# Performance work log

Hardware: AMD Instinct MI355X
Metric: run time of the kernel (lower is better)

## Reference

```python
import jax, jax.numpy as jnp
import numpy as np

EPS = 1e-5

def _rmsnorm(x, g):
    xf = x.astype(jnp.float32)
    rms = jnp.sqrt(jnp.mean(xf * xf + EPS, axis=-1, keepdims=True))
    return (xf / rms * g).astype(x.dtype)

def setup_inputs() -> dict:
    key = jax.random.key(0)
    ks = jax.random.split(key, 10)
    B, S, D, H, F = 2, 2048, 1024, 16, 4096
    s = 0.02
    return {
        "x": jax.random.normal(ks[0], (B, S, D), jnp.float32),
        "g1": jnp.ones((D,), jnp.float32),
        "wq": jax.random.normal(ks[1], (D, D), jnp.float32) * s,
        "wk": jax.random.normal(ks[2], (D, D), jnp.float32) * s,
        "wv": jax.random.normal(ks[3], (D, D), jnp.float32) * s,
        "wo": jax.random.normal(ks[4], (D, D), jnp.float32) * s,
        "g2": jnp.ones((D,), jnp.float32),
        "w1": jax.random.normal(ks[5], (F, D), jnp.float32) * s,
        "w2": jax.random.normal(ks[6], (D, F), jnp.float32) * s,
        "w3": jax.random.normal(ks[7], (F, D), jnp.float32) * s,
    }

def reference(x, g1, wq, wk, wv, wo, g2, w1, w2, w3):
    B, S, D = x.shape
    H = 16
    hd = D // H
    # --- attention sublayer ---
    xn = _rmsnorm(x, g1)
    q = jnp.einsum('bsd,ed->bse', xn, wq).reshape(B, S, H, hd).transpose(0, 2, 1, 3)
    k = jnp.einsum('bsd,ed->bse', xn, wk).reshape(B, S, H, hd).transpose(0, 2, 1, 3)
    v = jnp.einsum('bsd,ed->bse', xn, wv).reshape(B, S, H, hd).transpose(0, 2, 1, 3)
    scores = jnp.einsum('bhqd,bhkd->bhqk', q, k) / jnp.sqrt(jnp.float32(hd))
    mask = jnp.tril(jnp.ones((S, S), bool))  # causal
    neg = jnp.finfo(scores.dtype).min
    scores = jnp.where(mask[None, None], scores, neg)
    probs = jax.nn.softmax(scores, axis=-1)
    o = jnp.einsum('bhqk,bhkd->bhqd', probs, v)
    o = o.transpose(0, 2, 1, 3).reshape(B, S, D)
    attn_out = jnp.einsum('bsv,dv->bsd', o, wo)
    h = x + attn_out
    # --- SwiGLU sublayer ---
    hn = _rmsnorm(h, g2)
    p1 = jnp.einsum('fd,bsd->bsf', w1, hn)
    p3 = jnp.einsum('fd,bsd->bsf', w3, hn)
    ffn = jnp.einsum('df,bsf->bsd', w2, jax.nn.silu(p1) * p3)
    return h + ffn
```

## Files before the change

### kernel.cpp

```cpp
#include <hip/hip_runtime.h>

typedef __attribute__((ext_vector_type(8))) short short8;
typedef __attribute__((ext_vector_type(4))) float f32x4;

__device__ __forceinline__ unsigned short f2b(float f) {
  union { float f; unsigned u; } v; v.f = f;
  unsigned r = v.u + 0x7fffu + ((v.u >> 16) & 1u);
  return (unsigned short)(r >> 16);
}
__device__ __forceinline__ float b2f(unsigned short b) {
  union { unsigned u; float f; } v; v.u = ((unsigned)b) << 16; return v.f;
}

__device__ __forceinline__ void gload_lds16(const void* g, void* l) {
  __builtin_amdgcn_global_load_lds(
      (const __attribute__((address_space(1))) void*)g,
      (__attribute__((address_space(3))) void*)l, 16, 0, 0);
}

__global__ __launch_bounds__(256) void cvt_k(const float* __restrict__ s,
                                             unsigned short* __restrict__ d, int n4) {
  int i = blockIdx.x * 256 + threadIdx.x;
  if (i >= n4) return;
  float4 v = ((const float4*)s)[i];
  ushort4 o;
  o.x = f2b(v.x); o.y = f2b(v.y); o.z = f2b(v.z); o.w = f2b(v.w);
  ((ushort4*)d)[i] = o;
}

__global__ __launch_bounds__(256) void rmsnorm_k(const float* __restrict__ x,
                                                 const float* __restrict__ g,
                                                 unsigned short* __restrict__ out) {
  const int row = blockIdx.x, tid = threadIdx.x;
  const float4 v = ((const float4*)(x + (size_t)row * 1024))[tid];
  float ss = v.x*v.x + v.y*v.y + v.z*v.z + v.w*v.w;
  #pragma unroll
  for (int d = 32; d > 0; d >>= 1) ss += __shfl_down(ss, d);
  __shared__ float red[4];
  if ((tid & 63) == 0) red[tid >> 6] = ss;
  __syncthreads();
  const float tot = red[0] + red[1] + red[2] + red[3];
  const float sc = rsqrtf(tot * (1.0f/1024.0f) + 1e-5f);
  const float4 gg = ((const float4*)g)[tid];
  ushort4 o;
  o.x = f2b(v.x * sc * gg.x); o.y = f2b(v.y * sc * gg.y);
  o.z = f2b(v.z * sc * gg.z); o.w = f2b(v.w * sc * gg.w);
  ((ushort4*)(out + (size_t)row * 1024))[tid] = o;
}

__global__ __launch_bounds__(256) void gate_k(unsigned short* __restrict__ p13) {
  const size_t i = (size_t)blockIdx.x * 256 + threadIdx.x;
  const int r = (int)(i >> 9);
  const int fc = ((int)i & 511) * 8;
  unsigned short* p1 = p13 + (size_t)r * 8192 + fc;
  const unsigned short* p3 = p13 + (size_t)r * 8192 + 4096 + fc;
  ushort4 a0 = ((const ushort4*)p1)[0], a1 = ((const ushort4*)p1)[1];
  ushort4 b0 = ((const ushort4*)p3)[0], b1 = ((const ushort4*)p3)[1];
  unsigned short va[8] = {a0.x,a0.y,a0.z,a0.w,a1.x,a1.y,a1.z,a1.w};
  unsigned short vb[8] = {b0.x,b0.y,b0.z,b0.w,b1.x,b1.y,b1.z,b1.w};
  unsigned short vo[8];
  #pragma unroll
  for (int j = 0; j < 8; ++j) {
    float f1 = b2f(va[j]), f3 = b2f(vb[j]);
    float s = f1 / (1.0f + __expf(-f1));
    vo[j] = f2b(s * f3);
  }
  ushort4 o0 = {vo[0],vo[1],vo[2],vo[3]}, o1 = {vo[4],vo[5],vo[6],vo[7]};
  ((ushort4*)p1)[0] = o0; ((ushort4*)p1)[1] = o1;
}

template<int EPI>
__global__ __launch_bounds__(256) void gemm_bt(
    const unsigned short* __restrict__ A, const unsigned short* __restrict__ W,
    int N, int K, int lda,
    unsigned short* __restrict__ Cb, const float* __restrict__ res,
    float* __restrict__ Cf, int ldc)
{
  __shared__ unsigned short sA[4096];
  __shared__ unsigned short sB[4096];
  const int tid = threadIdx.x;
  const int w = tid >> 6, l = tid & 63;
  const int l15 = l & 15, l4 = l >> 4;
  const int bm = blockIdx.y * 128, bn = blockIdx.x * 128;
  const int wm = (w >> 1) * 64, wn = (w & 1) * 64;
  const int c0 = w * 128 + l;
  const int ra0 = c0 >> 2,        ka0 = (c0 & 3) * 8;
  const int ra1 = (c0 + 64) >> 2, ka1 = ((c0 + 64) & 3) * 8;
  const unsigned short* Ar0 = A + (size_t)(bm + ra0) * lda + ka0;
  const unsigned short* Ar1 = A + (size_t)(bm + ra1) * lda + ka1;
  const unsigned short* Wr0 = W + (size_t)(bn + ra0) * K + ka0;
  const unsigned short* Wr1 = W + (size_t)(bn + ra1) * K + ka1;
  f32x4 acc[4][4];
  const f32x4 z4 = {0.f, 0.f, 0.f, 0.f};
  #pragma unroll
  for (int i = 0; i < 4; ++i)
    #pragma unroll
    for (int j = 0; j < 4; ++j) acc[i][j] = z4;

  for (int kt = 0; kt < K; kt += 32) {
    gload_lds16(Ar0 + kt, &sA[w * 1024]);
    gload_lds16(Ar1 + kt, &sA[w * 1024 + 512]);
    gload_lds16(Wr0 + kt, &sB[w * 1024]);
    gload_lds16(Wr1 + kt, &sB[w * 1024 + 512]);
    __syncthreads();
    short8 af[4], bf[4];
    #pragma unroll
    for (int mi = 0; mi < 4; ++mi)
      af[mi] = *(const short8*)&sA[(wm + mi*16 + l15)*32 + l4*8];
    #pragma unroll
    for (int ni = 0; ni < 4; ++ni)
      bf[ni] = *(const short8*)&sB[(wn + ni*16 + l15)*32 + l4*8];
    #pragma unroll
    for (int mi = 0; mi < 4; ++mi)
      #pragma unroll
      for (int ni = 0; ni < 4; ++ni)
        acc[mi][ni] = __builtin_amdgcn_mfma_f32_16x16x32_bf16(af[mi], bf[ni], acc[mi][ni], 0, 0, 0);
    __syncthreads();
  }
  #pragma unroll
  for (int mi = 0; mi < 4; ++mi)
    #pragma unroll
    for (int ni = 0; ni < 4; ++ni) {
      const int row0 = bm + wm + mi*16 + l4*4;
      const int col  = bn + wn + ni*16 + l15;
      #pragma unroll
      for (int r = 0; r < 4; ++r) {
        const float v = acc[mi][ni][r];
        if (EPI == 0) {
          Cb[(size_t)(row0 + r) * ldc + col] = f2b(v);
        } else {
          const size_t o = (size_t)(row0 + r) * ldc + col;
          Cf[o] = res[o] + v;
        }
      }
    }
}

__global__ __launch_bounds__(256) void vtrans_k(const unsigned short* __restrict__ QKV,
                                                unsigned short* __restrict__ VT) {
  __shared__ unsigned short sT[4096];
  const int st = blockIdx.x, dt = blockIdx.y, b = blockIdx.z;
  const int tid = threadIdx.x;
  #pragma unroll
  for (int half = 0; half < 2; ++half) {
    const int c = tid + half * 256;
    const int r = c >> 3;
    const int ch = c & 7;
    const unsigned short* src =
        QKV + (size_t)(b*2048 + st*64 + r) * 3072 + 2048 + dt*64 + ch*8;
    short8 v = *(const short8*)src;
    *(short8*)&sT[r*64 + ((ch ^ ((r >> 3) & 7)) * 8)] = v;
  }
  __syncthreads();
  #pragma unroll
  for (int half = 0; half < 2; ++half) {
    const int c = tid + half * 256;
    const int od = c >> 3;
    const int oc = c & 7;
    unsigned short tmp[8];
    #pragma unroll
    for (int j = 0; j < 8; ++j) {
      const int srow = oc*8 + j;
      const int chunk = (od >> 3) ^ ((srow >> 3) & 7);
      tmp[j] = sT[srow*64 + chunk*8 + (od & 7)];
    }
    *(short8*)&VT[(size_t)(b*1024 + dt*64 + od) * 2048 + st*64 + oc*8] = *(short8*)tmp;
  }
}

__global__ __launch_bounds__(256) void attn_k(const unsigned short* __restrict__ QKV,
                                              const unsigned short* __restrict__ VT,
                                              unsigned short* __restrict__ Ob)
{
  const int LDQ = 3072;
  const int b = blockIdx.y >> 4, h = blockIdx.y & 15;
  const int qb = (15 - (int)blockIdx.x) * 128;
  const int tid = threadIdx.x;
  const int w = tid >> 6, l = tid & 63;
  const int l15 = l & 15, l4 = l >> 4;
  const int qw = qb + w * 32;
  const unsigned short* Qg  = QKV + (size_t)(b * 2048) * LDQ + h * 64;
  const unsigned short* Kg  = Qg + 1024;
  const unsigned short* VTg = VT + (size_t)(b * 1024 + h * 64) * 2048;

  __shared__ unsigned short sK[2][4096];
  __shared__ unsigned short sVT[2][4096];
  __shared__ unsigned short sP[4][2304];

  short8 qf[2][2];
  #pragma unroll
  for (int qt = 0; qt < 2; ++qt)
    #pragma unroll
    for (int hc = 0; hc < 2; ++hc)
      qf[qt][hc] = *(const short8*)&Qg[(size_t)(qw + qt*16 + l15) * LDQ + hc*32 + l4*8];

  const int rc0 = tid >> 3;
  const int ch0 = (tid & 7) ^ (rc0 & 7);
  const int rc1 = rc0 + 32;
  const unsigned short* Ks0 = Kg  + (size_t)rc0 * LDQ  + ch0 * 8;
  const unsigned short* Ks1 = Kg  + (size_t)rc1 * LDQ  + ch0 * 8;
  const unsigned short* Vs0 = VTg + (size_t)rc0 * 2048 + ch0 * 8;
  const unsigned short* Vs1 = VTg + (size_t)rc1 * 2048 + ch0 * 8;
  const int wun0 = w * 512;
  const int wun1 = 2048 + w * 512;

  f32x4 accO[2][4];
  float m_run[2][4], l_run[2][4];
  const f32x4 z4 = {0.f,0.f,0.f,0.f};
  #pragma unroll
  for (int qt = 0; qt < 2; ++qt) {
    #pragma unroll
    for (int dt = 0; dt < 4; ++dt) accO[qt][dt] = z4;
    #pragma unroll
    for (int r = 0; r < 4; ++r) { m_run[qt][r] = -1e30f; l_run[qt][r] = 0.f; }
  }

  const int ntB = (qb >> 6) + 2;
#define ASTAGE(buf, t) do { \
    const size_t ko = (size_t)(t) * 64 * LDQ; const int vo = (t) * 64; \
    gload_lds16(Ks0 + ko, &sK[buf][wun0]); \
    gload_lds16(Ks1 + ko, &sK[buf][wun1]); \
    gload_lds16(Vs0 + vo, &sVT[buf][wun0]); \
    gload_lds16(Vs1 + vo, &sVT[buf][wun1]); } while (0)

  ASTAGE(0, 0);
  __syncthreads();
  int cur = 0;
  for (int t = 0; t < ntB; ++t) {
    if (t + 1 < ntB) ASTAGE(cur ^ 1, t + 1);
    const int kv = t * 64;
    if (kv <= qw + 31) {
      const unsigned short* Kb = sK[cur];
      const unsigned short* Vb = sVT[cur];
      const int lim = qw + 31 - kv;
      f32x4 sAcc[2][4];
      #pragma unroll
      for (int qt = 0; qt < 2; ++qt)
        #pragma unroll
        for (int nt = 0; nt < 4; ++nt) sAcc[qt][nt] = z4;
      #pragma unroll
      for (int nt = 0; nt < 4; ++nt) {
        if (nt * 16 <= lim) {
          const int krow = nt*16 + l15;
          const short8 kf0 = *(const short8*)&Kb[krow*64 + ((l4 ^ (krow & 7)) * 8)];
          const short8 kf1 = *(const short8*)&Kb[krow*64 + (((4 + l4) ^ (krow & 7)) * 8)];
          #pragma unroll
          for (int qt = 0; qt < 2; ++qt) {
            sAcc[qt][nt] = __builtin_amdgcn_mfma_f32_16x16x32_bf16(qf[qt][0], kf0, sAcc[qt][nt], 0,0,0);
            sAcc[qt][nt] = __builtin_amdgcn_mfma_f32_16x16x32_bf16(qf[qt][1], kf1, sAcc[qt][nt], 0,0,0);
          }
        }
      }
      const bool bound = (kv + 63 > qw);
      #pragma unroll
      for (int qt = 0; qt < 2; ++qt) {
        float fac[4]; bool resc_any = false;
        #pragma unroll
        for (int r = 0; r < 4; ++r) {
          float sv[4];
          #pragma unroll
          for (int nt = 0; nt < 4; ++nt)
            sv[nt] = (nt * 16 <= lim) ? sAcc[qt][nt][r] * 0.125f : -1e30f;
          if (bound) {
            const int row = qt*16 + l4*4 + r;
            #pragma unroll
            for (int nt = 0; nt < 4; ++nt)
              if (kv + nt*16 + l15 > qw + row) sv[nt] = -1e30f;
          }
          float mx = fmaxf(fmaxf(sv[0], sv[1]), fmaxf(sv[2], sv[3]));
          mx = fmaxf(mx, __shfl_xor(mx, 1));
          mx = fmaxf(mx, __shfl_xor(mx, 2));
          mx = fmaxf(mx, __shfl_xor(mx, 4));
          mx = fmaxf(mx, __shfl_xor(mx, 8));
          const float mo = m_run[qt][r];
          const bool resc = mx > mo + 8.0f;
          const float mn = resc ? mx : mo;
          const float f = resc ? __expf(mo - mn) : 1.0f;
          fac[r] = f; resc_any |= resc;
          const float p0 = __expf(sv[0]-mn), p1 = __expf(sv[1]-mn);
          const float p2 = __expf(sv[2]-mn), p3 = __expf(sv[3]-mn);
          float rs = (p0+p1)+(p2+p3);
          rs += __shfl_xor(rs,1); rs += __shfl_xor(rs,2);
          rs += __shfl_xor(rs,4); rs += __shfl_xor(rs,8);
          l_run[qt][r] = l_run[qt][r]*f + rs;
          m_run[qt][r] = mn;
          const int prow = qt*16 + l4*4 + r;
          sP[w][prow*72      + l15] = f2b(p0);
          sP[w][prow*72 + 16 + l15] = f2b(p1);
          sP[w][prow*72 + 32 + l15] = f2b(p2);
          sP[w][prow*72 + 48 + l15] = f2b(p3);
        }
        if (__any(resc_any)) {
          #pragma unroll
          for (int dt = 0; dt < 4; ++dt)
            #pragma unroll
            for (int r = 0; r < 4; ++r)
              accO[qt][dt][r] *= fac[r];
        }
      }
      short8 pf[2][2];
      #pragma unroll
      for (int qt = 0; qt < 2; ++qt)
        #pragma unroll
        for (int kc = 0; kc < 2; ++kc)
          pf[qt][kc] = *(const short8*)&sP[w][(qt*16 + l15)*72 + kc*32 + l4*8];
      #pragma unroll
      for (int dt = 0; dt < 4; ++dt) {
        const int vrow = dt*16 + l15;
        const short8 vf0 = *(const short8*)&Vb[vrow*64 + ((l4 ^ (vrow & 7)) * 8)];
        const short8 vf1 = *(const short8*)&Vb[vrow*64 + (((4 + l4) ^ (vrow & 7)) * 8)];
        #pragma unroll
        for (int qt = 0; qt < 2; ++qt) {
          accO[qt][dt] = __builtin_amdgcn_mfma_f32_16x16x32_bf16(pf[qt][0], vf0, accO[qt][dt], 0,0,0);
          accO[qt][dt] = __builtin_amdgcn_mfma_f32_16x16x32_bf16(pf[qt][1], vf1, accO[qt][dt], 0,0,0);
        }
      }
    }
    __syncthreads();
    cur ^= 1;
  }
  #pragma unroll
  for (int qt = 0; qt < 2; ++qt)
    #pragma unroll
    for (int dt = 0; dt < 4; ++dt)
      #pragma unroll
      for (int r = 0; r < 4; ++r) {
        const int row = qw + qt*16 + l4*4 + r;
        const float ov = accO[qt][dt][r] / l_run[qt][r];
        Ob[(size_t)(b*2048 + row) * 1024 + h*64 + dt*16 + l15] = f2b(ov);
      }
}

extern "C" void kernel_launch(void* const* d_in, const int* in_sizes, int n_in,
                              void* d_out, int out_size, void* d_ws, size_t ws_size,
                              hipStream_t stream) {
  const float* x  = (const float*)d_in[0];
  const float* g1 = (const float*)d_in[1];
  const float* wq = (const float*)d_in[2];
  const float* wk = (const float*)d_in[3];
  const float* wv = (const float*)d_in[4];
  const float* wo = (const float*)d_in[5];
  const float* g2 = (const float*)d_in[6];
  const float* w1 = (const float*)d_in[7];
  const float* w2 = (const float*)d_in[8];
  const float* w3 = (const float*)d_in[9];
  float* out = (float*)d_out;
  char* ws = (char*)d_ws;
  (void)in_sizes; (void)n_in; (void)out_size; (void)ws_size;

  unsigned short* Wqkv = (unsigned short*)(ws + 0);
  unsigned short* Wo   = (unsigned short*)(ws + 6291456);
  unsigned short* W13  = (unsigned short*)(ws + 8388608);
  unsigned short* W2   = (unsigned short*)(ws + 25165824);
  unsigned short* XN   = (unsigned short*)(ws + 33554432);
  unsigned short* QKV  = (unsigned short*)(ws + 41943040);
  unsigned short* OB   = (unsigned short*)(ws + 67108864);
  unsigned short* VTb  = (unsigned short*)(ws + 75497472);
  unsigned short* P13  = (unsigned short*)(ws + 41943040);
  float*          H    = (float*)(ws + 109051904);

  cvt_k<<<1024, 256, 0, stream>>>(wq, Wqkv,             262144);
  cvt_k<<<1024, 256, 0, stream>>>(wk, Wqkv + 1048576,   262144);
  cvt_k<<<1024, 256, 0, stream>>>(wv, Wqkv + 2097152,   262144);
  cvt_k<<<1024, 256, 0, stream>>>(wo, Wo,               262144);
  cvt_k<<<4096, 256, 0, stream>>>(w1, W13,             1048576);
  cvt_k<<<4096, 256, 0, stream>>>(w3, W13 + 4194304,   1048576);
  cvt_k<<<4096, 256, 0, stream>>>(w2, W2,              1048576);

  rmsnorm_k<<<4096, 256, 0, stream>>>(x, g1, XN);
  gemm_bt<0><<<dim3(24, 32), 256, 0, stream>>>(XN, Wqkv, 3072, 1024, 1024,
                                               QKV, nullptr, nullptr, 3072);
  vtrans_k<<<dim3(32, 16, 2), 256, 0, stream>>>(QKV, VTb);
  attn_k<<<dim3(16, 32), 256, 0, stream>>>(QKV, VTb, OB);
  gemm_bt<1><<<dim3(8, 32), 256, 0, stream>>>(OB, Wo, 1024, 1024, 1024,
                                              nullptr, x, H, 1024);
  rmsnorm_k<<<4096, 256, 0, stream>>>(H, g2, XN);
  gemm_bt<0><<<dim3(64, 32), 256, 0, stream>>>(XN, W13, 8192, 1024, 1024,
                                               P13, nullptr, nullptr, 8192);
  gate_k<<<8192, 256, 0, stream>>>(P13);
  gemm_bt<1><<<dim3(8, 32), 256, 0, stream>>>(P13, W2, 1024, 4096, 8192,
                                              nullptr, H, out, 1024);
}
```

Before: 571.1 us.

## Add 256x256-tile 4-stage pipelined bf16 GEMM for QKV and W1/W3 projections

```diff
diff --git a/kernel.cpp b/kernel.cpp
--- a/kernel.cpp
+++ b/kernel.cpp
@@ -134,6 +134,113 @@
         }
       }
     }
+}
+
+__global__ __launch_bounds__(512, 2) void gemm256_bt(
+    const unsigned short* __restrict__ A, const unsigned short* __restrict__ W,
+    int K, int lda, unsigned short* __restrict__ Cb, int ldc, int nbx)
+{
+  __shared__ unsigned short sA[4][8192];
+  __shared__ unsigned short sB[4][8192];
+  const int tid = threadIdx.x;
+  const int w = tid >> 6, l = tid & 63;
+  const int l15 = l & 15, l4 = l >> 4;
+  const int nwg = nbx * gridDim.y;
+  const int flat = blockIdx.y * nbx + blockIdx.x;
+  const int q8 = nwg >> 3;
+  const int sw = (flat & 7) * q8 + (flat >> 3);
+  const int bm = (sw / nbx) * 256, bn = (sw % nbx) * 256;
+
+  int rowl[2], coll[2];
+  #pragma unroll
+  for (int i = 0; i < 2; ++i) {
+    const int g = w * 128 + i * 64 + l;
+    const int s = g >> 6, j = g & 63;
+    const int r = j >> 2, c8 = (j & 3) * 8;
+    rowl[i] = s * 16 + r;
+    coll[i] = c8 ^ ((r & 8) << 1);
+  }
+  const unsigned short* As0 = A + (size_t)(bm + rowl[0]) * lda + coll[0];
+  const unsigned short* As1 = A + (size_t)(bm + rowl[1]) * lda + coll[1];
+  const unsigned short* Ws0 = W + (size_t)(bn + rowl[0]) * K + coll[0];
+  const unsigned short* Ws1 = W + (size_t)(bn + rowl[1]) * K + coll[1];
+  const int d0 = w * 1024, d1 = w * 1024 + 512;
+
+  const int swzr = (l4 * 8) ^ ((l15 & 8) << 1);
+  const int aoff = (w >> 2) * 4096 + l15 * 32 + swzr;
+  const int boff = (w & 3) * 2048 + l15 * 32 + swzr;
+
+  f32x4 acc[8][4];
+  const f32x4 z4 = {0.f, 0.f, 0.f, 0.f};
+  #pragma unroll
+  for (int i = 0; i < 8; ++i)
+    #pragma unroll
+    for (int j = 0; j < 4; ++j) acc[i][j] = z4;
+
+  const int NT = K >> 5;
+  #pragma unroll
+  for (int p = 0; p < 3; ++p) {
+    const int ko = p * 32;
+    gload_lds16(As0 + ko, &sA[p][d0]);
+    gload_lds16(As1 + ko, &sA[p][d1]);
+    gload_lds16(Ws0 + ko, &sB[p][d0]);
+    gload_lds16(Ws1 + ko, &sB[p][d1]);
+  }
+  asm volatile("s_waitcnt vmcnt(8)" ::: "memory");
+  __builtin_amdgcn_s_barrier();
+
+  for (int t = 0; t < NT; ++t) {
+    const unsigned short* a_ = sA[t & 3];
+    const unsigned short* b_ = sB[t & 3];
+    const bool st = (t + 3 < NT);
+    const int nb = (t + 3) & 3;
+    const int ko = (t + 3) * 32;
+    short8 bfr[4], afr[4];
+    #pragma unroll
+    for (int ni = 0; ni < 4; ++ni) bfr[ni] = *(const short8*)&b_[boff + ni * 512];
+    #pragma unroll
+    for (int mi = 0; mi < 4; ++mi) afr[mi] = *(const short8*)&a_[aoff + mi * 512];
+    if (st) { gload_lds16(As0 + ko, &sA[nb][d0]); gload_lds16(Ws0 + ko, &sB[nb][d0]); }
+    __builtin_amdgcn_s_barrier();
+    asm volatile("s_waitcnt lgkmcnt(0)" ::: "memory");
+    __builtin_amdgcn_sched_barrier(0);
+    __builtin_amdgcn_s_setprio(1);
+    #pragma unroll
+    for (int mi = 0; mi < 4; ++mi)
+      #pragma unroll
+      for (int ni = 0; ni < 4; ++ni)
+        acc[mi][ni] = __builtin_amdgcn_mfma_f32_16x16x32_bf16(bfr[ni], afr[mi], acc[mi][ni], 0, 0, 0);
+    __builtin_amdgcn_s_setprio(0);
+    __builtin_amdgcn_s_barrier();
+    #pragma unroll
+    for (int mi = 0; mi < 4; ++mi) afr[mi] = *(const short8*)&a_[aoff + (mi + 4) * 512];
+    if (st) { gload_lds16(As1 + ko, &sA[nb][d1]); gload_lds16(Ws1 + ko, &sB[nb][d1]); }
+    __builtin_amdgcn_s_barrier();
+    asm volatile("s_waitcnt lgkmcnt(0)" ::: "memory");
+    __builtin_amdgcn_sched_barrier(0);
+    __builtin_amdgcn_s_setprio(1);
+    #pragma unroll
+    for (int mi = 0; mi < 4; ++mi)
+      #pragma unroll
+      for (int ni = 0; ni < 4; ++ni)
+        acc[mi + 4][ni] = __builtin_amdgcn_mfma_f32_16x16x32_bf16(bfr[ni], afr[mi], acc[mi + 4][ni], 0, 0, 0);
+    __builtin_amdgcn_s_setprio(0);
+    if (t < NT - 3)       asm volatile("s_waitcnt vmcnt(8)" ::: "memory");
+    else if (t == NT - 3) asm volatile("s_waitcnt vmcnt(4)" ::: "memory");
+    else                  asm volatile("s_waitcnt vmcnt(0)" ::: "memory");
+    __builtin_amdgcn_s_barrier();
+  }
+  #pragma unroll
+  for (int mi = 0; mi < 8; ++mi) {
+    const int row = bm + (w >> 2) * 128 + mi * 16 + l15;
+    #pragma unroll
+    for (int ni = 0; ni < 4; ++ni) {
+      const int col = bn + (w & 3) * 64 + ni * 16 + l4 * 4;
+      ushort4 o = { f2b(acc[mi][ni][0]), f2b(acc[mi][ni][1]),
+                    f2b(acc[mi][ni][2]), f2b(acc[mi][ni][3]) };
+      *(ushort4*)&Cb[(size_t)row * ldc + col] = o;
+    }
+  }
 }
 
 __global__ __launch_bounds__(256) void vtrans_k(const unsigned short* __restrict__ QKV,
@@ -368,15 +475,13 @@
   cvt_k<<<4096, 256, 0, stream>>>(w2, W2,              1048576);
 
   rmsnorm_k<<<4096, 256, 0, stream>>>(x, g1, XN);
-  gemm_bt<0><<<dim3(24, 32), 256, 0, stream>>>(XN, Wqkv, 3072, 1024, 1024,
-                                               QKV, nullptr, nullptr, 3072);
+  gemm256_bt<<<dim3(12, 16), 512, 0, stream>>>(XN, Wqkv, 1024, 1024, QKV, 3072, 12);
   vtrans_k<<<dim3(32, 16, 2), 256, 0, stream>>>(QKV, VTb);
   attn_k<<<dim3(16, 32), 256, 0, stream>>>(QKV, VTb, OB);
   gemm_bt<1><<<dim3(8, 32), 256, 0, stream>>>(OB, Wo, 1024, 1024, 1024,
                                               nullptr, x, H, 1024);
   rmsnorm_k<<<4096, 256, 0, stream>>>(H, g2, XN);
-  gemm_bt<0><<<dim3(64, 32), 256, 0, stream>>>(XN, W13, 8192, 1024, 1024,
-                                               P13, nullptr, nullptr, 8192);
+  gemm256_bt<<<dim3(32, 16), 512, 0, stream>>>(XN, W13, 1024, 1024, P13, 8192, 32);
   gate_k<<<8192, 256, 0, stream>>>(P13);
   gemm_bt<1><<<dim3(8, 32), 256, 0, stream>>>(P13, W2, 1024, 4096, 8192,
                                               nullptr, H, out, 1024);
```

New measurement: 569.1 us. Within noise of the previous version (-0.4%).
